# Performance work log

Measured on AMD Instinct MI355X. Metric: run time of the kernel, lower is better.

The kernel has to match this reference:

```python
import jax, jax.numpy as jnp
import numpy as np

INTERVAL = 0.02

def setup_inputs() -> dict:
    key = jax.random.key(0)
    ks = jax.random.split(key, 10)
    B, N, D, F = 8, 256, 64, 64
    return {
        "rbf_0": jax.random.normal(ks[0], (B, N, N, D), jnp.float32),
        "rbf_d": jax.random.normal(ks[1], (B, N, N, D), jnp.float32),
        "Q0_w": jax.random.normal(ks[2], (F, D), jnp.float32) * 0.1,
        "Q0_b": jax.random.normal(ks[3], (F,), jnp.float32) * 0.1,
        "Q_w": jax.random.normal(ks[4], (F, D), jnp.float32) * 0.1,
        "Q_b": jax.random.normal(ks[5], (F,), jnp.float32) * 0.1,
        "R0_w": jax.random.normal(ks[6], (F, D), jnp.float32) * 0.1,
        "R0_b": jax.random.normal(ks[7], (F,), jnp.float32) * 0.1,
        "R_w": jax.random.normal(ks[8], (F, D), jnp.float32) * 0.1,
        "R_b": jax.random.normal(ks[9], (F,), jnp.float32) * 0.1,
    }

def _linear(x, w, b):
    # x: [..., D], w: [F, D], b: [F] -> [..., F]
    return jnp.einsum('...d,fd->...f', x, w) + b

def reference(rbf_0, rbf_d, Q0_w, Q0_b, Q_w, Q_b, R0_w, R0_b, R_w, R_b):
    q_0 = _linear(rbf_0, Q0_w, Q0_b)   # [B, N, N, F]
    q = _linear(rbf_d, Q_w, Q_b)       # [B, N, N, F]
    r_0 = _linear(rbf_0, R0_w, R0_b)   # [B, N, N, F]
    r = _linear(rbf_d, R_w, R_b)       # [B, N, N, F]
    # 3-index correlator: contract over i and f
    C = jnp.einsum('bnif,bijf->bnj', q_0 * q, r_0 * r) * INTERVAL
    return C
```

## Files before the change

### kernel.cpp

```cpp
#include <hip/hip_runtime.h>
#include <hip/hip_bf16.h>


typedef __bf16 bf16x8 __attribute__((ext_vector_type(8)));
typedef float  f32x4  __attribute__((ext_vector_type(4)));
typedef int    i32x4  __attribute__((ext_vector_type(4)));
typedef unsigned short u16;
typedef u16    u16x8  __attribute__((ext_vector_type(8)));

static __device__ __forceinline__ __bf16 f2bf(float x) {
  union { __hip_bfloat16 h; __bf16 b; } u;
  u.h = __float2bfloat16(x);
  return u.b;
}
static __device__ __forceinline__ u16 f2bfu(float x) {
  union { __hip_bfloat16 h; u16 s; } u;
  u.h = __float2bfloat16(x);
  return u.s;
}
static __device__ __forceinline__ float bfu2f(u16 s) {
  union { unsigned int u; float f; } v;
  v.u = ((unsigned int)s) << 16;
  return v.f;
}
static __device__ __forceinline__ void gload16_nt(const float* gsrc, float* ldst) {
  __builtin_amdgcn_global_load_lds(
      (const __attribute__((address_space(1))) void*)gsrc,
      (__attribute__((address_space(3))) void*)ldst, 16, 0, 2);
}

__global__ __launch_bounds__(256, 3) void k_phase1(
    const float* __restrict__ rbf0, const float* __restrict__ rbfd,
    const float* __restrict__ Q0w, const float* __restrict__ Q0b,
    const float* __restrict__ Qw,  const float* __restrict__ Qb,
    const float* __restrict__ R0w, const float* __restrict__ R0b,
    const float* __restrict__ Rw,  const float* __restrict__ Rb,
    u16* __restrict__ Aout, u16* __restrict__ Bout)
{
  __shared__ __align__(16) float lds[3][2][2048];

  const int tid  = threadIdx.x;
  const int lane = tid & 63;
  const int wave = tid >> 6;
  const int fr   = lane & 15;
  const int kg   = lane >> 4;
  const int role = wave >> 1;
  const int s    = wave & 1;

  const float* W0 = role ? R0w : Q0w;
  const float* W1 = role ? Rw  : Qw;
  const float* B0 = role ? R0b : Q0b;
  const float* B1 = role ? Rb  : Qb;
  u16* __restrict__ Out = role ? Bout : Aout;

  bf16x8 wf0[2][4], wf1[2][4];
#pragma unroll
  for (int kt = 0; kt < 2; ++kt)
#pragma unroll
    for (int ft = 0; ft < 4; ++ft) {
      const float* p0 = W0 + (ft * 16 + fr) * 64 + kt * 32 + kg * 8;
      const float* p1 = W1 + (ft * 16 + fr) * 64 + kt * 32 + kg * 8;
      f32x4 a = *(const f32x4*)p0, b = *(const f32x4*)(p0 + 4);
      f32x4 c = *(const f32x4*)p1, d = *(const f32x4*)(p1 + 4);
      bf16x8 w0v, w1v;
#pragma unroll
      for (int j = 0; j < 4; ++j) {
        w0v[j] = f2bf(a[j]); w0v[j + 4] = f2bf(b[j]);
        w1v[j] = f2bf(c[j]); w1v[j + 4] = f2bf(d[j]);
      }
      wf0[kt][ft] = w0v; wf1[kt][ft] = w1v;
    }

  u16x8 pb0[2], pb1[2];
#pragma unroll
  for (int ft = 0; ft < 4; ++ft)
#pragma unroll
    for (int r = 0; r < 4; ++r) {
      int idx = ft * 4 + r;
      pb0[idx >> 3][idx & 7] = f2bfu(B0[ft * 16 + kg * 4 + r]);
      pb1[idx >> 3][idx & 7] = f2bfu(B1[ft * 16 + kg * 4 + r]);
    }

  const int g0 = tid, g1 = 256 + tid;
  const int c0 = ((g0 >> 4) << 4) | ((g0 & 15) ^ ((g0 >> 4) & 15));
  const int c1 = ((g1 >> 4) << 4) | ((g1 & 15) ^ ((g1 >> 4) & 15));
  const int f0 = c0 * 4, f1 = c1 * 4;
  const int d0 = wave * 256, d1 = (wave + 4) * 256;

  const int bt0 = blockIdx.x;

#define S1_ISSUE(IT, SET)                                              \
  {                                                                    \
    const float* b0_ = rbf0 + (size_t)(bt0 + (IT) * 2048) * 2048;      \
    const float* b1_ = rbfd + (size_t)(bt0 + (IT) * 2048) * 2048;      \
    gload16_nt(b0_ + f0, &lds[SET][0][d0]);                            \
    gload16_nt(b0_ + f1, &lds[SET][0][d1]);                            \
    gload16_nt(b1_ + f0, &lds[SET][1][d0]);                            \
    gload16_nt(b1_ + f1, &lds[SET][1][d1]);                            \
  }

#define S1_COMPUTE(IT, SET)                                            \
  {                                                                    \
    const int row = s * 16 + fr;                     \
    f32x4 ra[4], rb[4];                                                \
    _Pragma("unroll")                                                  \
    for (int kt = 0; kt < 2; ++kt)                                     \
      _Pragma("unroll")                                                \
      for (int h = 0; h < 2; ++h) {                                    \
        int c = kt * 8 + kg * 2 + h;                                   \
        int chunk = (row << 4) | (c ^ fr);                             \
        ra[kt * 2 + h] = *(const f32x4*)&lds[SET][0][chunk * 4];       \
        rb[kt * 2 + h] = *(const f32x4*)&lds[SET][1][chunk * 4];       \
      }                                                                \
    bf16x8 x0f[2], xdf[2];                                             \
    _Pragma("unroll")                                                  \
    for (int kt = 0; kt < 2; ++kt)                                     \
      _Pragma("unroll")                                                \
      for (int j = 0; j < 4; ++j) {                                    \
        x0f[kt][j]     = f2bf(ra[kt * 2][j]);                          \
        x0f[kt][j + 4] = f2bf(ra[kt * 2 + 1][j]);                      \
        xdf[kt][j]     = f2bf(rb[kt * 2][j]);                          \
        xdf[kt][j + 4] = f2bf(rb[kt * 2 + 1][j]);                      \
      }                                                                \
    f32x4 acc0[4], acc1[4];                                            \
    _Pragma("unroll")                                                  \
    for (int ft = 0; ft < 4; ++ft)                                     \
      _Pragma("unroll")                                                \
      for (int r = 0; r < 4; ++r) {                                    \
        int idx = ft * 4 + r;                                          \
        acc0[ft][r] = bfu2f(pb0[idx >> 3][idx & 7]);                   \
        acc1[ft][r] = bfu2f(pb1[idx >> 3][idx & 7]);                   \
      }                                                                \
    _Pragma("unroll")                                                  \
    for (int kt = 0; kt < 2; ++kt)                                     \
      _Pragma("unroll")                                                \
      for (int ft = 0; ft < 4; ++ft) {                                 \
        acc0[ft] = __builtin_amdgcn_mfma_f32_16x16x32_bf16(            \
            wf0[kt][ft], x0f[kt], acc0[ft], 0, 0, 0);                  \
        acc1[ft] = __builtin_amdgcn_mfma_f32_16x16x32_bf16(            \
            wf1[kt][ft], xdf[kt], acc1[ft], 0, 0, 0);                  \
      }                                                                \
    u16x8 o0, o1;                                                      \
    _Pragma("unroll")                                                  \
    for (int ft = 0; ft < 4; ++ft)                                     \
      _Pragma("unroll")                                                \
      for (int r = 0; r < 4; ++r) {                                    \
        int idx = ft * 4 + r;                                          \
        float v = acc0[ft][r] * acc1[ft][r];                           \
        if (idx < 8) o0[idx & 7] = f2bfu(v); else o1[idx & 7] = f2bfu(v); \
      }                                                                \
    u16* dst = Out + ((size_t)((bt0 + (IT) * 2048) * 32 + s * 16 + fr)) * 64 + kg * 16; \
    *(u16x8*)dst       = o0;                                           \
    *(u16x8*)(dst + 8) = o1;                                           \
  }

#define S1_ITER(IT, NWAIT, DO_ISSUE)                                   \
  {                                                                    \
    if (DO_ISSUE) S1_ISSUE((IT) + 2, ((IT) + 2) % 3);                  \
    asm volatile("s_waitcnt vmcnt(" #NWAIT ")" ::: "memory");          \
    __builtin_amdgcn_s_barrier();                                      \
    __builtin_amdgcn_sched_barrier(0);                                 \
    S1_COMPUTE(IT, (IT) % 3);                                          \
    asm volatile("s_waitcnt lgkmcnt(0)" ::: "memory");                 \
    __builtin_amdgcn_s_barrier();                                      \
    __builtin_amdgcn_sched_barrier(0);                                 \
  }

  S1_ISSUE(0, 0);
  S1_ISSUE(1, 1);

  S1_ITER(0,  8, 1);
  S1_ITER(1, 10, 1);
  S1_ITER(2, 12, 1);
  S1_ITER(3, 12, 1);
  S1_ITER(4, 12, 1);
  S1_ITER(5, 12, 1);
  S1_ITER(6,  8, 0);
  S1_ITER(7,  4, 0);

#undef S1_ITER
#undef S1_COMPUTE
#undef S1_ISSUE
}

__global__ __launch_bounds__(256, 2) void k_phase2(
    const u16* __restrict__ A, const u16* __restrict__ Bm,
    float* __restrict__ C)
{
  __shared__ __align__(16) u16 Alds[128 * 64];
  __shared__ __align__(16) u16 Blds[128 * 64];

  const int tid  = threadIdx.x;
  const int lane = tid & 63;
  const int wave = tid >> 6;
  const int fr   = lane & 15;
  const int kg   = lane >> 4;

  const int bid = blockIdx.x;
  const int kc = bid & 15;
  const int jt = (bid >> 4) & 1;
  const int nt = (bid >> 5) & 1;
  const int b  = bid >> 6;
  const int n0 = nt * 128, j0 = jt * 128;
  const int wr = wave >> 1, wc = wave & 1;

  const u16* Ab = A  + (size_t)b * 4194304;
  const u16* Bb = Bm + (size_t)b * 4194304;

  f32x4 acc[4][4];
#pragma unroll
  for (int mt = 0; mt < 4; ++mt)
#pragma unroll
    for (int nn = 0; nn < 4; ++nn) {
      acc[mt][nn][0] = 0.f; acc[mt][nn][1] = 0.f; acc[mt][nn][2] = 0.f; acc[mt][nn][3] = 0.f;
    }

  for (int ii = 0; ii < 16; ++ii) {
    const int i = kc * 16 + ii;

    i32x4 va[4], vb[4];
#pragma unroll
    for (int rep = 0; rep < 4; ++rep) {
      int c = tid + rep * 256;
      int row = c >> 3, ch = c & 7;
      va[rep] = *(const i32x4*)(Ab + (size_t)(n0 + row) * 16384 + (size_t)i * 64 + ch * 8);
      vb[rep] = *(const i32x4*)(Bb + (size_t)i * 16384 + (size_t)(j0 + row) * 64 + ch * 8);
    }
    __syncthreads();
#pragma unroll
    for (int rep = 0; rep < 4; ++rep) {
      int c = tid + rep * 256;
      int row = c >> 3, ch = c & 7;
      int sw = ch ^ (row & 7);
      *(i32x4*)&Alds[row * 64 + sw * 8] = va[rep];
      *(i32x4*)&Blds[row * 64 + sw * 8] = vb[rep];
    }
    __syncthreads();

#pragma unroll
    for (int ks = 0; ks < 2; ++ks) {
      bf16x8 af[4], bfv[4];
#pragma unroll
      for (int mt = 0; mt < 4; ++mt) {
        int row = wr * 64 + mt * 16 + fr;
        int sw = (ks * 4 + kg) ^ (row & 7);
        af[mt] = *(const bf16x8*)&Alds[row * 64 + sw * 8];
      }
#pragma unroll
      for (int nn = 0; nn < 4; ++nn) {
        int row = wc * 64 + nn * 16 + fr;
        int sw = (ks * 4 + kg) ^ (row & 7);
        bfv[nn] = *(const bf16x8*)&Blds[row * 64 + sw * 8];
      }
#pragma unroll
      for (int mt = 0; mt < 4; ++mt)
#pragma unroll
        for (int nn = 0; nn < 4; ++nn)
          acc[mt][nn] = __builtin_amdgcn_mfma_f32_16x16x32_bf16(af[mt], bfv[nn], acc[mt][nn], 0, 0, 0);
    }
  }

  float* Cb = C + ((size_t)b << 16);
#pragma unroll
  for (int mt = 0; mt < 4; ++mt)
#pragma unroll
    for (int nn = 0; nn < 4; ++nn)
#pragma unroll
      for (int r = 0; r < 4; ++r) {
        int n = n0 + wr * 64 + mt * 16 + kg * 4 + r;
        int j = j0 + wc * 64 + nn * 16 + fr;
        atomicAdd(&Cb[n * 256 + j], acc[mt][nn][r] * 0.02f);
      }
}

extern "C" void kernel_launch(void* const* d_in, const int* in_sizes, int n_in,
                              void* d_out, int out_size, void* d_ws, size_t ws_size,
                              hipStream_t stream)
{
  const float* rbf0 = (const float*)d_in[0];
  const float* rbfd = (const float*)d_in[1];
  const float* Q0w  = (const float*)d_in[2];
  const float* Q0b  = (const float*)d_in[3];
  const float* Qw   = (const float*)d_in[4];
  const float* Qb   = (const float*)d_in[5];
  const float* R0w  = (const float*)d_in[6];
  const float* R0b  = (const float*)d_in[7];
  const float* Rw   = (const float*)d_in[8];
  const float* Rb   = (const float*)d_in[9];
  float* out = (float*)d_out;

  u16* Abuf = (u16*)d_ws;
  u16* Bbuf = Abuf + (size_t)33554432;

  hipMemsetAsync(d_out, 0, (size_t)out_size * sizeof(float), stream);
  hipLaunchKernelGGL(k_phase1, dim3(2048), dim3(256), 0, stream,
                     rbf0, rbfd, Q0w, Q0b, Qw, Qb, R0w, R0b, Rw, Rb, Abuf, Bbuf);
  hipLaunchKernelGGL(k_phase2, dim3(512), dim3(256), 0, stream, Abuf, Bbuf, out);
}
```

Before: 141.8 us.

## Restructure phase2 into 1024-thread full-tile blocks with async double-buffered LDS loads

Phase 2 now runs 256 blocks of 1024 threads. Each block owns the full 256x256 output tile for one batch and an 8-wide slice of i, instead of 512 blocks of 128x128 tiles over 16 i values. Operand staging moves from register loads plus LDS stores to direct global-to-LDS loads, double-buffered and overlapped with MFMA compute using explicit waitcnt and barriers. This removes register round-trips and duplicate A/B reads across output tiles. In exchange there are fewer blocks, twice as many atomic adds to the output from the finer i split, and heavier barrier synchronisation.

```diff
diff --git a/kernel.cpp b/kernel.cpp
--- a/kernel.cpp
+++ b/kernel.cpp
@@ -27,6 +27,11 @@
   __builtin_amdgcn_global_load_lds(
       (const __attribute__((address_space(1))) void*)gsrc,
       (__attribute__((address_space(3))) void*)ldst, 16, 0, 2);
+}
+static __device__ __forceinline__ void gload16u(const u16* gsrc, u16* ldst) {
+  __builtin_amdgcn_global_load_lds(
+      (const __attribute__((address_space(1))) void*)gsrc,
+      (__attribute__((address_space(3))) void*)ldst, 16, 0, 0);
 }
 
 __global__ __launch_bounds__(256, 3) void k_phase1(
@@ -101,7 +106,7 @@
 
 #define S1_COMPUTE(IT, SET)                                            \
   {                                                                    \
-    const int row = s * 16 + fr;                     \
+    const int row = s * 16 + fr;                                       \
     f32x4 ra[4], rb[4];                                                \
     _Pragma("unroll")                                                  \
     for (int kt = 0; kt < 2; ++kt)                                     \
@@ -183,82 +188,108 @@
 #undef S1_ISSUE
 }
 
-__global__ __launch_bounds__(256, 2) void k_phase2(
+__global__ __launch_bounds__(1024, 4) void k_phase2(
     const u16* __restrict__ A, const u16* __restrict__ Bm,
     float* __restrict__ C)
 {
-  __shared__ __align__(16) u16 Alds[128 * 64];
-  __shared__ __align__(16) u16 Blds[128 * 64];
+  __shared__ __align__(16) u16 As[2][16384];
+  __shared__ __align__(16) u16 Bs[2][16384];
 
   const int tid  = threadIdx.x;
   const int lane = tid & 63;
   const int wave = tid >> 6;
   const int fr   = lane & 15;
   const int kg   = lane >> 4;
+  const int wr   = wave >> 2;
+  const int wc   = wave & 3;
 
   const int bid = blockIdx.x;
-  const int kc = bid & 15;
-  const int jt = (bid >> 4) & 1;
-  const int nt = (bid >> 5) & 1;
-  const int b  = bid >> 6;
-  const int n0 = nt * 128, j0 = jt * 128;
-  const int wr = wave >> 1, wc = wave & 1;
+  const int kc  = bid & 31;
+  const int b   = bid >> 5;
+  const int i0  = kc * 8;
 
   const u16* Ab = A  + (size_t)b * 4194304;
   const u16* Bb = Bm + (size_t)b * 4194304;
 
+  const int gA0 = wave * 64 + lane, gA1 = 1024 + gA0;
+  const int r0 = gA0 >> 3, ch0 = gA0 & 7, cs0 = ch0 ^ (r0 & 7);
+  const int r1 = gA1 >> 3, ch1 = gA1 & 7, cs1 = ch1 ^ (r1 & 7);
+  const int rowA0 = r0 * 16384 + cs0 * 8;
+  const int rowA1 = r1 * 16384 + cs1 * 8;
+  const int rowB0 = r0 * 64 + cs0 * 8;
+  const int rowB1 = r1 * 64 + cs1 * 8;
+  const int dst0 = (wave * 64) * 8;
+  const int dst1 = (1024 + wave * 64) * 8;
+
   f32x4 acc[4][4];
 #pragma unroll
   for (int mt = 0; mt < 4; ++mt)
 #pragma unroll
     for (int nn = 0; nn < 4; ++nn) {
-      acc[mt][nn][0] = 0.f; acc[mt][nn][1] = 0.f; acc[mt][nn][2] = 0.f; acc[mt][nn][3] = 0.f;
+      acc[mt][nn][0] = 0.f; acc[mt][nn][1] = 0.f;
+      acc[mt][nn][2] = 0.f; acc[mt][nn][3] = 0.f;
     }
 
-  for (int ii = 0; ii < 16; ++ii) {
-    const int i = kc * 16 + ii;
-
-    i32x4 va[4], vb[4];
-#pragma unroll
-    for (int rep = 0; rep < 4; ++rep) {
-      int c = tid + rep * 256;
-      int row = c >> 3, ch = c & 7;
-      va[rep] = *(const i32x4*)(Ab + (size_t)(n0 + row) * 16384 + (size_t)i * 64 + ch * 8);
-      vb[rep] = *(const i32x4*)(Bb + (size_t)i * 16384 + (size_t)(j0 + row) * 64 + ch * 8);
-    }
-    __syncthreads();
-#pragma unroll
-    for (int rep = 0; rep < 4; ++rep) {
-      int c = tid + rep * 256;
-      int row = c >> 3, ch = c & 7;
-      int sw = ch ^ (row & 7);
-      *(i32x4*)&Alds[row * 64 + sw * 8] = va[rep];
-      *(i32x4*)&Blds[row * 64 + sw * 8] = vb[rep];
-    }
-    __syncthreads();
-
-#pragma unroll
-    for (int ks = 0; ks < 2; ++ks) {
-      bf16x8 af[4], bfv[4];
-#pragma unroll
-      for (int mt = 0; mt < 4; ++mt) {
-        int row = wr * 64 + mt * 16 + fr;
-        int sw = (ks * 4 + kg) ^ (row & 7);
-        af[mt] = *(const bf16x8*)&Alds[row * 64 + sw * 8];
-      }
-#pragma unroll
-      for (int nn = 0; nn < 4; ++nn) {
-        int row = wc * 64 + nn * 16 + fr;
-        int sw = (ks * 4 + kg) ^ (row & 7);
-        bfv[nn] = *(const bf16x8*)&Blds[row * 64 + sw * 8];
-      }
-#pragma unroll
-      for (int mt = 0; mt < 4; ++mt)
-#pragma unroll
-        for (int nn = 0; nn < 4; ++nn)
-          acc[mt][nn] = __builtin_amdgcn_mfma_f32_16x16x32_bf16(af[mt], bfv[nn], acc[mt][nn], 0, 0, 0);
-    }
-  }
+#define S2_ISSUE(I, BUF)                                               \
+  {                                                                    \
+    gload16u(Ab + rowA0 + (I) * 64, &As[BUF][dst0]);                   \
+    gload16u(Ab + rowA1 + (I) * 64, &As[BUF][dst1]);                   \
+    gload16u(Bb + rowB0 + (size_t)(I) * 16384, &Bs[BUF][dst0]);        \
+    gload16u(Bb + rowB1 + (size_t)(I) * 16384, &Bs[BUF][dst1]);        \
+  }
+
+#define S2_COMPUTE(BUF)                                                \
+  {                                                                    \
+    _Pragma("unroll")                                                  \
+    for (int kt = 0; kt < 2; ++kt) {                                   \
+      bf16x8 af[4], bfv[4];                                            \
+      _Pragma("unroll")                                                \
+      for (int mt = 0; mt < 4; ++mt) {                                 \
+        int row = wr * 64 + mt * 16 + fr;                              \
+        int c = kt * 4 + kg;                                           \
+        af[mt] = *(const bf16x8*)&As[BUF][row * 64 + ((c ^ (row & 7)) * 8)]; \
+      }                                                                \
+      _Pragma("unroll")                                                \
+      for (int nn = 0; nn < 4; ++nn) {                                 \
+        int row = wc * 64 + nn * 16 + fr;                              \
+        int c = kt * 4 + kg;                                           \
+        bfv[nn] = *(const bf16x8*)&Bs[BUF][row * 64 + ((c ^ (row & 7)) * 8)]; \
+      }                                                                \
+      _Pragma("unroll")                                                \
+      for (int mt = 0; mt < 4; ++mt)                                   \
+        _Pragma("unroll")                                              \
+        for (int nn = 0; nn < 4; ++nn)                                 \
+          acc[mt][nn] = __builtin_amdgcn_mfma_f32_16x16x32_bf16(       \
+              af[mt], bfv[nn], acc[mt][nn], 0, 0, 0);                  \
+    }                                                                  \
+  }
+
+#define S2_ITER(IT, NWAIT, DO_ISSUE)                                   \
+  {                                                                    \
+    if (DO_ISSUE) S2_ISSUE(i0 + (IT) + 1, ((IT) + 1) & 1);             \
+    asm volatile("s_waitcnt vmcnt(" #NWAIT ")" ::: "memory");          \
+    __builtin_amdgcn_s_barrier();                                      \
+    __builtin_amdgcn_sched_barrier(0);                                 \
+    S2_COMPUTE((IT) & 1);                                              \
+    asm volatile("s_waitcnt lgkmcnt(0)" ::: "memory");                 \
+    __builtin_amdgcn_s_barrier();                                      \
+    __builtin_amdgcn_sched_barrier(0);                                 \
+  }
+
+  S2_ISSUE(i0, 0);
+
+  S2_ITER(0, 4, 1);
+  S2_ITER(1, 4, 1);
+  S2_ITER(2, 4, 1);
+  S2_ITER(3, 4, 1);
+  S2_ITER(4, 4, 1);
+  S2_ITER(5, 4, 1);
+  S2_ITER(6, 4, 1);
+  S2_ITER(7, 0, 0);
+
+#undef S2_ITER
+#undef S2_COMPUTE
+#undef S2_ISSUE
 
   float* Cb = C + ((size_t)b << 16);
 #pragma unroll
@@ -267,8 +298,8 @@
     for (int nn = 0; nn < 4; ++nn)
 #pragma unroll
       for (int r = 0; r < 4; ++r) {
-        int n = n0 + wr * 64 + mt * 16 + kg * 4 + r;
-        int j = j0 + wc * 64 + nn * 16 + fr;
+        int n = wr * 64 + mt * 16 + kg * 4 + r;
+        int j = wc * 64 + nn * 16 + fr;
         atomicAdd(&Cb[n * 256 + j], acc[mt][nn][r] * 0.02f);
       }
 }
@@ -295,5 +326,5 @@
   hipMemsetAsync(d_out, 0, (size_t)out_size * sizeof(float), stream);
   hipLaunchKernelGGL(k_phase1, dim3(2048), dim3(256), 0, stream,
                      rbf0, rbfd, Q0w, Q0b, Qw, Qb, R0w, R0b, Rw, Rb, Abuf, Bbuf);
-  hipLaunchKernelGGL(k_phase2, dim3(512), dim3(256), 0, stream, Abuf, Bbuf, out);
-}
+  hipLaunchKernelGGL(k_phase2, dim3(256), dim3(1024), 0, stream, Abuf, Bbuf, out);
+}
```

After: 169.4 us. +19.5%, slower.
